# Optimization experiments

Measured on AMD Instinct MI355X. Metric: run time of the kernel, lower is better.

Reference implementation:

```python
import jax, jax.numpy as jnp
import numpy as np


def setup_inputs() -> dict:
    key = jax.random.key(0)
    ks = jax.random.split(key, 8)
    B, C, H, W = 8, 512, 64, 64
    Cr = C // 8  # reduction=8
    s = 1.0 / np.sqrt(C)
    return {
        "x": jax.random.normal(ks[0], (B, C, H, W), jnp.float32),
        "wq": jax.random.normal(ks[1], (Cr, C), jnp.float32) * s,
        "bq": jax.random.normal(ks[2], (Cr,), jnp.float32) * 0.01,
        "wk": jax.random.normal(ks[3], (Cr, C), jnp.float32) * s,
        "bk": jax.random.normal(ks[4], (Cr,), jnp.float32) * 0.01,
        "wv": jax.random.normal(ks[5], (C, C), jnp.float32) * s,
        "bv": jax.random.normal(ks[6], (C,), jnp.float32) * 0.01,
        "gamma": jax.random.normal(ks[7], (1,), jnp.float32),
    }


def reference(x, wq, bq, wk, bk, wv, bv, gamma):
    B, C, H, W = x.shape
    N = H * W
    xf = x.reshape(B, C, N)  # 1x1 conv == channel matmul
    q = jnp.einsum('qc,bcn->bnq', wq, xf) + bq  # [B, N, Cr]
    k = jnp.einsum('qc,bcn->bqn', wk, xf) + bk[None, :, None]  # [B, Cr, N]
    v = jnp.einsum('vc,bcn->bvn', wv, xf) + bv[None, :, None]  # [B, C, N]
    energy = jnp.einsum('bnq,bqm->bnm', q, k)  # [B, N, N]
    attn = jax.nn.softmax(energy, axis=-1)
    out = jnp.einsum('bcm,bnm->bcn', v, attn)  # [B, C, N]
    out = out.reshape(B, C, H, W)
    return gamma * out + x
```

## Files before the change

### kernel.cpp

```cpp
#include <hip/hip_runtime.h>

typedef float  f32x4  __attribute__((ext_vector_type(4)));
typedef float  f32x16 __attribute__((ext_vector_type(16)));
typedef short  short8 __attribute__((ext_vector_type(8)));
typedef unsigned int uint4v __attribute__((ext_vector_type(4)));

#define LOG2E 1.4426950408889634f
#define NPIX 4096
#define CCH  512
#define DQK  64

__device__ __forceinline__ ushort f2b(float f) {
  union { float f; unsigned u; } v; v.f = f;
  unsigned r = v.u + 0x7fffu + ((v.u >> 16) & 1u);
  return (ushort)(r >> 16);
}

__device__ __forceinline__ unsigned cvt_pk_bf16(float lo, float hi) {
  unsigned r;
  asm("v_cvt_pk_bf16_f32 %0, %1, %2" : "=v"(r) : "v"(lo), "v"(hi));
  return r;
}

__device__ __forceinline__ void plane_swap(unsigned &a, unsigned &b) {
  asm volatile("v_permlane32_swap_b32 %0, %1" : "+v"(a), "+v"(b));
}

__global__ __launch_bounds__(256) void k_cast_x(const float* __restrict__ x,
                                                ushort* __restrict__ Xt) {
  __shared__ float tile[32][33];
  const int b = blockIdx.z;
  const int n0 = blockIdx.x * 32, c0 = blockIdx.y * 32;
  const int t = threadIdx.x;
  {
    int cc = t >> 3, nn = (t & 7) * 4;
    const float4 v = *(const float4*)&x[((size_t)b * CCH + c0 + cc) * NPIX + n0 + nn];
    tile[cc][nn] = v.x; tile[cc][nn + 1] = v.y; tile[cc][nn + 2] = v.z; tile[cc][nn + 3] = v.w;
  }
  __syncthreads();
  {
    int nr = t >> 3, c4 = (t & 7) * 4;
    ushort4 o;
    o.x = f2b(tile[c4 + 0][nr]); o.y = f2b(tile[c4 + 1][nr]);
    o.z = f2b(tile[c4 + 2][nr]); o.w = f2b(tile[c4 + 3][nr]);
    *(ushort4*)&Xt[((size_t)b * NPIX + n0 + nr) * CCH + c0 + c4] = o;
  }
}

__global__ __launch_bounds__(256) void k_cast_w(const float* __restrict__ wq,
                                                const float* __restrict__ wk,
                                                const float* __restrict__ wv,
                                                ushort* __restrict__ Wb) {
  int i = blockIdx.x * 256 + threadIdx.x;
  int idx = i * 4;
  int j = idx >> 9, c = idx & 511;
  const float* src = (j < 64) ? &wq[(size_t)j * 512]
                   : (j < 128) ? &wk[(size_t)(j - 64) * 512]
                               : &wv[(size_t)(j - 128) * 512];
  float4 v = *(const float4*)&src[c];
  ushort4 o; o.x = f2b(v.x); o.y = f2b(v.y); o.z = f2b(v.z); o.w = f2b(v.w);
  *(ushort4*)&Wb[idx] = o;
}

__global__ __launch_bounds__(256) void k_proj(const ushort* __restrict__ Xt,
                                              const ushort* __restrict__ Wb,
                                              const float* __restrict__ bq,
                                              const float* __restrict__ bk,
                                              const float* __restrict__ bv,
                                              ushort* __restrict__ Q,
                                              ushort* __restrict__ Kf,
                                              ushort* __restrict__ Vf) {
  __shared__ ushort Wl[64][72];
  __shared__ ushort Xl[64][72];
  const int b = blockIdx.z;
  const int n0 = blockIdx.x * 64;
  const int j0 = blockIdx.y * 64;
  const int t = threadIdx.x;
  const int w = t >> 6, l = t & 63;
  const int lr = l & 15, lq = l >> 4;
  const int wj = (w >> 1) * 32, wn = (w & 1) * 32;

  f32x4 acc[2][2];
#pragma unroll
  for (int a = 0; a < 2; ++a)
#pragma unroll
    for (int c = 0; c < 2; ++c) acc[a][c] = f32x4{0.f, 0.f, 0.f, 0.f};

  const int srow = t >> 2, sch = t & 3;
  for (int k0 = 0; k0 < 512; k0 += 64) {
    *(uint4*)&Wl[srow][sch * 8]       = *(const uint4*)&Wb[(size_t)(j0 + srow) * 512 + k0 + sch * 8];
    *(uint4*)&Wl[srow][(sch + 4) * 8] = *(const uint4*)&Wb[(size_t)(j0 + srow) * 512 + k0 + (sch + 4) * 8];
    *(uint4*)&Xl[srow][sch * 8]       = *(const uint4*)&Xt[((size_t)b * NPIX + n0 + srow) * 512 + k0 + sch * 8];
    *(uint4*)&Xl[srow][(sch + 4) * 8] = *(const uint4*)&Xt[((size_t)b * NPIX + n0 + srow) * 512 + k0 + (sch + 4) * 8];
    __syncthreads();
#pragma unroll
    for (int kt = 0; kt < 2; ++kt) {
      short8 af[2], bf[2];
#pragma unroll
      for (int jt = 0; jt < 2; ++jt)
        af[jt] = *(const short8*)&Wl[wj + jt * 16 + lr][kt * 32 + lq * 8];
#pragma unroll
      for (int nt = 0; nt < 2; ++nt)
        bf[nt] = *(const short8*)&Xl[wn + nt * 16 + lr][kt * 32 + lq * 8];
#pragma unroll
      for (int jt = 0; jt < 2; ++jt)
#pragma unroll
        for (int nt = 0; nt < 2; ++nt)
          acc[jt][nt] = __builtin_amdgcn_mfma_f32_16x16x32_bf16(af[jt], bf[nt], acc[jt][nt], 0, 0, 0);
    }
    __syncthreads();
  }

#pragma unroll
  for (int jt = 0; jt < 2; ++jt) {
    const int jb = j0 + wj + jt * 16;
#pragma unroll
    for (int nt = 0; nt < 2; ++nt) {
      const int n = n0 + wn + nt * 16 + lr;
      const size_t nrow = (size_t)b * NPIX + n;
      const int n32 = (n0 + wn) >> 5;
      if (jb < 64) {
        ushort4 o;
        o.x = f2b(LOG2E * (acc[jt][nt][0] + bq[jb + lq * 4 + 0]));
        o.y = f2b(LOG2E * (acc[jt][nt][1] + bq[jb + lq * 4 + 1]));
        o.z = f2b(LOG2E * (acc[jt][nt][2] + bq[jb + lq * 4 + 2]));
        o.w = f2b(LOG2E * (acc[jt][nt][3] + bq[jb + lq * 4 + 3]));
        *(ushort4*)&Q[nrow * DQK + jb + lq * 4] = o;
      } else if (jb < 128) {
        const int kd0 = jb - 64 + lq * 4;
        const int ks = (jb - 64) >> 4;
        const int hl = lq >> 1;
        const int e0 = (lq * 4) & 7;
        const int lp = (nt * 16 + lr) + 32 * hl;
        ushort4 o;
        o.x = f2b(acc[jt][nt][0] + bk[kd0 + 0]);
        o.y = f2b(acc[jt][nt][1] + bk[kd0 + 1]);
        o.z = f2b(acc[jt][nt][2] + bk[kd0 + 2]);
        o.w = f2b(acc[jt][nt][3] + bk[kd0 + 3]);
        *(ushort4*)&Kf[((size_t)(b * 128 + n32) * 4 + ks) * 512 + lp * 8 + e0] = o;
      } else {
        const int kt = nt;
        const int hlv = (lr >> 3) & 1;
        const int e = lr & 7;
#pragma unroll
        for (int r = 0; r < 4; ++r) {
          const int c = jb - 128 + lq * 4 + r;
          Vf[(((size_t)(b * 128 + n32) * 16 + (c >> 5)) * 2 + kt) * 512 +
             (c & 31) * 8 + 256 * hlv + e] = f2b(acc[jt][nt][r] + bv[c]);
        }
      }
    }
  }
}

__global__ __launch_bounds__(512, 4) void k_attn(const ushort* __restrict__ Qb,
                                                 const ushort* __restrict__ Kf,
                                                 const ushort* __restrict__ Vf,
                                                 const float* __restrict__ x,
                                                 const float* __restrict__ gamma,
                                                 float* __restrict__ out) {
  __shared__ unsigned Plds[2][8][2][2][64][2];
  __shared__ float Lred[2][4][32];
  const int id = blockIdx.x;
  const int b  = id & 7;
  const int qb = id >> 3;
  const int t = threadIdx.x;
  const int w = t >> 6, l = t & 63;
  const int lq = l & 31, h = l >> 5;
  const int kg = w >> 1;
  const int q32p = w & 1;
  const int qw = qb * 64;

  union PB { uint4v u; short8 s8; };

  const ushort* qptr  = Qb + ((size_t)b * NPIX + qw + q32p * 32 + lq) * DQK + h * 8;
  const ushort* kbase = Kf + (size_t)b * 128 * 2048 + (size_t)l * 8;
  const ushort* vbase = Vf + (size_t)b * 128 * 16384 + (size_t)(2 * w) * 1024 + (size_t)l * 8;

  f32x16 acc[2][2] = {};
  float Lp = 0.f;

  for (int tile = 0; tile < 32; ++tile) {
    const int buf = tile & 1;

    {
      const ushort* pk_ = kbase + (size_t)(tile * 4 + kg) * 2048;
      short8 kf0 = *(const short8*)(pk_);
      short8 kf1 = *(const short8*)(pk_ + 512);
      short8 kf2 = *(const short8*)(pk_ + 1024);
      short8 kf3 = *(const short8*)(pk_ + 1536);
      short8 q0 = *(const short8*)(qptr);
      short8 q1 = *(const short8*)(qptr + 16);
      short8 q2 = *(const short8*)(qptr + 32);
      short8 q3 = *(const short8*)(qptr + 48);
      f32x16 s = {};
      __builtin_amdgcn_s_setprio(1);
      s = __builtin_amdgcn_mfma_f32_32x32x16_bf16(kf0, q0, s, 0, 0, 0);
      s = __builtin_amdgcn_mfma_f32_32x32x16_bf16(kf1, q1, s, 0, 0, 0);
      s = __builtin_amdgcn_mfma_f32_32x32x16_bf16(kf2, q2, s, 0, 0, 0);
      s = __builtin_amdgcn_mfma_f32_32x32x16_bf16(kf3, q3, s, 0, 0, 0);
      __builtin_amdgcn_s_setprio(0);

      float sum = 0.f;
#pragma unroll
      for (int r = 0; r < 16; ++r) { s[r] = __builtin_amdgcn_exp2f(s[r]); sum += s[r]; }
      Lp += sum;
      unsigned pk0 = cvt_pk_bf16(s[0],  s[1]),  pk1 = cvt_pk_bf16(s[2],  s[3]);
      unsigned pk2 = cvt_pk_bf16(s[4],  s[5]),  pk3 = cvt_pk_bf16(s[6],  s[7]);
      unsigned pk4 = cvt_pk_bf16(s[8],  s[9]),  pk5 = cvt_pk_bf16(s[10], s[11]);
      unsigned pk6 = cvt_pk_bf16(s[12], s[13]), pk7 = cvt_pk_bf16(s[14], s[15]);
      plane_swap(pk0, pk2); plane_swap(pk1, pk3);
      plane_swap(pk4, pk6); plane_swap(pk5, pk7);
      *(uint2*)&Plds[buf][kg * 2 + 0][q32p][0][l][0] = uint2{pk0, pk1};
      *(uint2*)&Plds[buf][kg * 2 + 0][q32p][1][l][0] = uint2{pk2, pk3};
      *(uint2*)&Plds[buf][kg * 2 + 1][q32p][0][l][0] = uint2{pk4, pk5};
      *(uint2*)&Plds[buf][kg * 2 + 1][q32p][1][l][0] = uint2{pk6, pk7};
    }
    __syncthreads();

#pragma unroll
    for (int k8 = 0; k8 < 8; ++k8) {
      const ushort* pv = vbase + (size_t)(tile * 4 + (k8 >> 1)) * 16384 + (size_t)(k8 & 1) * 512;
      short8 v0 = *(const short8*)(pv);
      short8 v1 = *(const short8*)(pv + 1024);
      uint2 a0 = *(const uint2*)&Plds[buf][k8][0][0][l][0];
      uint2 a1 = *(const uint2*)&Plds[buf][k8][0][1][l][0];
      uint2 b0 = *(const uint2*)&Plds[buf][k8][1][0][l][0];
      uint2 b1 = *(const uint2*)&Plds[buf][k8][1][1][l][0];
      PB B0, B1;
      B0.u[0] = a0.x; B0.u[1] = a0.y; B0.u[2] = a1.x; B0.u[3] = a1.y;
      B1.u[0] = b0.x; B1.u[1] = b0.y; B1.u[2] = b1.x; B1.u[3] = b1.y;
      __builtin_amdgcn_s_setprio(1);
      acc[0][0] = __builtin_amdgcn_mfma_f32_32x32x16_bf16(v0, B0.s8, acc[0][0], 0, 0, 0);
      acc[0][1] = __builtin_amdgcn_mfma_f32_32x32x16_bf16(v1, B0.s8, acc[0][1], 0, 0, 0);
      acc[1][0] = __builtin_amdgcn_mfma_f32_32x32x16_bf16(v0, B1.s8, acc[1][0], 0, 0, 0);
      acc[1][1] = __builtin_amdgcn_mfma_f32_32x32x16_bf16(v1, B1.s8, acc[1][1], 0, 0, 0);
      __builtin_amdgcn_s_setprio(0);
    }
  }

  Lp += __shfl_xor(Lp, 32);
  Lred[q32p][kg][lq] = Lp;
  __syncthreads();
  float Lt0 = (Lred[0][0][lq] + Lred[0][1][lq]) + (Lred[0][2][lq] + Lred[0][3][lq]);
  float Lt1 = (Lred[1][0][lq] + Lred[1][1][lq]) + (Lred[1][2][lq] + Lred[1][3][lq]);
  const float g = gamma[0];
  const float gi0 = g / Lt0, gi1 = g / Lt1;
#pragma unroll
  for (int ct = 0; ct < 2; ++ct)
#pragma unroll
    for (int r = 0; r < 16; ++r) {
      const int c = w * 64 + ct * 32 + (r & 3) + 8 * (r >> 2) + 4 * h;
      const size_t base = ((size_t)b * CCH + c) * NPIX + qw + lq;
      out[base]      = gi0 * acc[0][ct][r] + x[base];
      out[base + 32] = gi1 * acc[1][ct][r] + x[base + 32];
    }
}

extern "C" void kernel_launch(void* const* d_in, const int* in_sizes, int n_in,
                              void* d_out, int out_size, void* d_ws, size_t ws_size,
                              hipStream_t stream) {
  const float* x     = (const float*)d_in[0];
  const float* wq    = (const float*)d_in[1];
  const float* bq    = (const float*)d_in[2];
  const float* wk    = (const float*)d_in[3];
  const float* bk    = (const float*)d_in[4];
  const float* wv    = (const float*)d_in[5];
  const float* bv    = (const float*)d_in[6];
  const float* gamma = (const float*)d_in[7];
  float* out = (float*)d_out;

  ushort* Xt = (ushort*)d_out;
  ushort* Wb = (ushort*)d_ws;
  ushort* Qb = Wb + (size_t)640 * 512;
  ushort* Kf = Qb + (size_t)8 * NPIX * DQK;
  ushort* Vf = Kf + (size_t)8 * 128 * 4 * 512;

  k_cast_x<<<dim3(NPIX / 32, CCH / 32, 8), 256, 0, stream>>>(x, Xt);
  k_cast_w<<<(640 * 512 / 4) / 256, 256, 0, stream>>>(wq, wk, wv, Wb);
  k_proj<<<dim3(NPIX / 64, 640 / 64, 8), 256, 0, stream>>>(Xt, Wb, bq, bk, bv, Qb, Kf, Vf);
  k_attn<<<dim3(512), 512, 0, stream>>>(Qb, Kf, Vf, x, gamma, out);
}
```

Before: 255.8 us.

## Stage K and Q tiles in LDS via async global_load_lds double buffering

The attention kernel now copies each K tile into a double-buffered LDS region with direct global-to-LDS loads, prefetching the next tile while the current one is computed. Q is loaded once into LDS. The projection kernel writes Q in the same MFMA fragment layout already used for K. Before, each wave read K fragments straight from global memory, and the four wave pairs sharing a kg re-read the same data; staging is meant to cut that redundant global traffic and hide its latency. The cost is about 40KB more LDS per block, which may lower occupancy, and correctness depends on the existing barriers in the unseen loop body ordering buffer reuse.

```diff
diff --git a/kernel.cpp b/kernel.cpp
--- a/kernel.cpp
+++ b/kernel.cpp
@@ -24,6 +24,11 @@
 
 __device__ __forceinline__ void plane_swap(unsigned &a, unsigned &b) {
   asm volatile("v_permlane32_swap_b32 %0, %1" : "+v"(a), "+v"(b));
+}
+
+__device__ __forceinline__ void gload16(const ushort* g, ushort* l) {
+  __builtin_amdgcn_global_load_lds((const __attribute__((address_space(1))) void*)g,
+                                   (__attribute__((address_space(3))) void*)l, 16, 0, 0);
 }
 
 __global__ __launch_bounds__(256) void k_cast_x(const float* __restrict__ x,
@@ -67,7 +72,7 @@
                                               const float* __restrict__ bq,
                                               const float* __restrict__ bk,
                                               const float* __restrict__ bv,
-                                              ushort* __restrict__ Q,
+                                              ushort* __restrict__ Qf,
                                               ushort* __restrict__ Kf,
                                               ushort* __restrict__ Vf) {
   __shared__ ushort Wl[64][72];
@@ -117,15 +122,19 @@
 #pragma unroll
     for (int nt = 0; nt < 2; ++nt) {
       const int n = n0 + wn + nt * 16 + lr;
-      const size_t nrow = (size_t)b * NPIX + n;
       const int n32 = (n0 + wn) >> 5;
       if (jb < 64) {
+        const int kd0 = jb + lq * 4;
+        const int ks = jb >> 4;
+        const int hl = lq >> 1;
+        const int e0 = (lq * 4) & 7;
+        const int lp = (nt * 16 + lr) + 32 * hl;
         ushort4 o;
-        o.x = f2b(LOG2E * (acc[jt][nt][0] + bq[jb + lq * 4 + 0]));
-        o.y = f2b(LOG2E * (acc[jt][nt][1] + bq[jb + lq * 4 + 1]));
-        o.z = f2b(LOG2E * (acc[jt][nt][2] + bq[jb + lq * 4 + 2]));
-        o.w = f2b(LOG2E * (acc[jt][nt][3] + bq[jb + lq * 4 + 3]));
-        *(ushort4*)&Q[nrow * DQK + jb + lq * 4] = o;
+        o.x = f2b(LOG2E * (acc[jt][nt][0] + bq[kd0 + 0]));
+        o.y = f2b(LOG2E * (acc[jt][nt][1] + bq[kd0 + 1]));
+        o.z = f2b(LOG2E * (acc[jt][nt][2] + bq[kd0 + 2]));
+        o.w = f2b(LOG2E * (acc[jt][nt][3] + bq[kd0 + 3]));
+        *(ushort4*)&Qf[((size_t)(b * 128 + n32) * 4 + ks) * 512 + lp * 8 + e0] = o;
       } else if (jb < 128) {
         const int kd0 = jb - 64 + lq * 4;
         const int ks = (jb - 64) >> 4;
@@ -153,13 +162,15 @@
   }
 }
 
-__global__ __launch_bounds__(512, 4) void k_attn(const ushort* __restrict__ Qb,
+__global__ __launch_bounds__(512, 4) void k_attn(const ushort* __restrict__ Qf,
                                                  const ushort* __restrict__ Kf,
                                                  const ushort* __restrict__ Vf,
                                                  const float* __restrict__ x,
                                                  const float* __restrict__ gamma,
                                                  float* __restrict__ out) {
   __shared__ unsigned Plds[2][8][2][2][64][2];
+  __shared__ ushort Klds[2][8192];
+  __shared__ ushort Qlds[4096];
   __shared__ float Lred[2][4][32];
   const int id = blockIdx.x;
   const int b  = id & 7;
@@ -173,26 +184,40 @@
 
   union PB { uint4v u; short8 s8; };
 
-  const ushort* qptr  = Qb + ((size_t)b * NPIX + qw + q32p * 32 + lq) * DQK + h * 8;
-  const ushort* kbase = Kf + (size_t)b * 128 * 2048 + (size_t)l * 8;
-  const ushort* vbase = Vf + (size_t)b * 128 * 16384 + (size_t)(2 * w) * 1024 + (size_t)l * 8;
+  const ushort* kslice = Kf + (size_t)(b * 128) * 2048;
+  const ushort* vbase  = Vf + (size_t)b * 128 * 16384 + (size_t)(2 * w) * 1024 + (size_t)l * 8;
 
   f32x16 acc[2][2] = {};
   float Lp = 0.f;
 
+  auto stageK = [&](int buf, int tile) {
+    const ushort* src = kslice + (size_t)tile * 8192;
+#pragma unroll
+    for (int i = 0; i < 2; ++i) {
+      const int cb_ = i * 512 + w * 64;
+      gload16(src + (size_t)(cb_ + l) * 8, &Klds[buf][cb_ * 8]);
+    }
+  };
+
+  gload16(Qf + (size_t)(b * 128 + qb * 2) * 2048 + (size_t)(w * 64 + l) * 8, &Qlds[w * 512]);
+  stageK(0, 0);
+  __syncthreads();
+
   for (int tile = 0; tile < 32; ++tile) {
     const int buf = tile & 1;
+    if (tile + 1 < 32) stageK(buf ^ 1, tile + 1);
 
     {
-      const ushort* pk_ = kbase + (size_t)(tile * 4 + kg) * 2048;
-      short8 kf0 = *(const short8*)(pk_);
-      short8 kf1 = *(const short8*)(pk_ + 512);
-      short8 kf2 = *(const short8*)(pk_ + 1024);
-      short8 kf3 = *(const short8*)(pk_ + 1536);
-      short8 q0 = *(const short8*)(qptr);
-      short8 q1 = *(const short8*)(qptr + 16);
-      short8 q2 = *(const short8*)(qptr + 32);
-      short8 q3 = *(const short8*)(qptr + 48);
+      const ushort* kb = &Klds[buf][(kg * 4) * 512 + l * 8];
+      short8 kf0 = *(const short8*)(kb);
+      short8 kf1 = *(const short8*)(kb + 512);
+      short8 kf2 = *(const short8*)(kb + 1024);
+      short8 kf3 = *(const short8*)(kb + 1536);
+      const ushort* qp = &Qlds[q32p * 2048 + l * 8];
+      short8 q0 = *(const short8*)(qp);
+      short8 q1 = *(const short8*)(qp + 512);
+      short8 q2 = *(const short8*)(qp + 1024);
+      short8 q3 = *(const short8*)(qp + 1536);
       f32x16 s = {};
       __builtin_amdgcn_s_setprio(1);
       s = __builtin_amdgcn_mfma_f32_32x32x16_bf16(kf0, q0, s, 0, 0, 0);
@@ -272,12 +297,12 @@
 
   ushort* Xt = (ushort*)d_out;
   ushort* Wb = (ushort*)d_ws;
-  ushort* Qb = Wb + (size_t)640 * 512;
-  ushort* Kf = Qb + (size_t)8 * NPIX * DQK;
+  ushort* Qf = Wb + (size_t)640 * 512;
+  ushort* Kf = Qf + (size_t)8 * 128 * 4 * 512;
   ushort* Vf = Kf + (size_t)8 * 128 * 4 * 512;
 
   k_cast_x<<<dim3(NPIX / 32, CCH / 32, 8), 256, 0, stream>>>(x, Xt);
   k_cast_w<<<(640 * 512 / 4) / 256, 256, 0, stream>>>(wq, wk, wv, Wb);
-  k_proj<<<dim3(NPIX / 64, 640 / 64, 8), 256, 0, stream>>>(Xt, Wb, bq, bk, bv, Qb, Kf, Vf);
-  k_attn<<<dim3(512), 512, 0, stream>>>(Qb, Kf, Vf, x, gamma, out);
-}
+  k_proj<<<dim3(NPIX / 64, 640 / 64, 8), 256, 0, stream>>>(Xt, Wb, bq, bk, bv, Qf, Kf, Vf);
+  k_attn<<<dim3(512), 512, 0, stream>>>(Qf, Kf, Vf, x, gamma, out);
+}
```

New measurement: 255.6 us. About the same (-0.0%).
